# Kernel tuning notes

Measured on AMD Instinct MI355X. Metric: run time of the kernel, lower is better.

Reference implementation:

```python
import jax, jax.numpy as jnp
import numpy as np

N_TOKEN = 267735
D_EMBED = 1024
D_PROJ = 1024
DIV_VAL = 4
CUTOFFS = [20000, 40000, 200000, N_TOKEN]   # cutoffs + [n_token]
ENDS = [0] + CUTOFFS                         # cutoff_ends
N_CLUSTERS = len(CUTOFFS) - 1                # 3
HEAD_SIZE = CUTOFFS[0] + N_CLUSTERS          # 20003
N = 1024                                     # len*bsz


def setup_inputs() -> dict:
    key = jax.random.key(0)
    ks = jax.random.split(key, 16)
    d_embs = [D_EMBED // DIV_VAL ** i for i in range(4)]  # 1024,256,64,16
    sizes = [HEAD_SIZE] + [ENDS[i + 1] - ENDS[i] for i in range(1, 4)]  # 20003,20000,160000,67735
    s = 0.02
    inp = {
        'hidden': jax.random.normal(ks[0], (N, D_PROJ), dtype=jnp.float32),
        'target': jax.random.randint(ks[1], (N,), 0, N_TOKEN, dtype=jnp.int32),
    }
    for i in range(4):
        inp[f'w{i}'] = jax.random.normal(ks[2 + 3 * i], (sizes[i], d_embs[i]), dtype=jnp.float32) * s
        inp[f'b{i}'] = jnp.zeros((sizes[i],), dtype=jnp.float32)
        inp[f'p{i}'] = jax.random.normal(ks[3 + 3 * i], (D_PROJ, d_embs[i]), dtype=jnp.float32) * s
    return inp


def _logit(h, w, b, p):
    # F.linear(hidden, proj.t()) -> h @ p ; F.linear(., weight, bias) -> @ w.T + b
    return (h @ p) @ w.T + b


def reference(hidden, target, w0, b0, p0, w1, b1, p1, w2, b2, p2, w3, b3, p3):
    head_lp = jax.nn.log_softmax(_logit(hidden, w0, b0, p0), axis=1)  # [N, HEAD_SIZE]
    tails = [(w1, b1, p1), (w2, b2, p2), (w3, b3, p3)]
    lps = []
    # shortlist cluster: gather target logprob directly from head
    t0 = jnp.clip(target, 0, CUTOFFS[0] - 1)
    lps.append(jnp.take_along_axis(head_lp, t0[:, None], axis=1)[:, 0])
    # tail clusters: small projected matmul + log_softmax + gather, combined with cluster logprob head_lp[:, -i]
    for i in range(1, 4):
        l, r = ENDS[i], ENDS[i + 1]
        ti = jnp.clip(target - l, 0, r - l - 1)
        tail_lp = jax.nn.log_softmax(_logit(hidden, *tails[i - 1]), axis=1)  # [N, r-l]
        lps.append(head_lp[:, -i] + jnp.take_along_axis(tail_lp, ti[:, None], axis=1)[:, 0])
    masks = [(target >= ENDS[i]) & (target < ENDS[i + 1]) for i in range(4)]
    logprob = jnp.select(masks, lps)
    return -logprob  # [N] per-token NLL, original order (keep_order=True)
```

## Files before the change

### kernel.cpp

```cpp
#include <hip/hip_runtime.h>
#include <hip/hip_bf16.h>
#include <math.h>

#define NTOK 1024
#define DPROJ 1024
#define PSTRIDE 1376
#define HEADS 20003
#define LOG2E 1.4426950408889634f
#define LN2   0.6931471805599453f
#define WSCALE (4.0f * LOG2E)
#define PSCALE 0.25f

typedef __attribute__((ext_vector_type(8))) short bf16x8;
typedef __attribute__((ext_vector_type(4))) float f32x4;
typedef long long i64;

__device__ __forceinline__ short f2bf(float f) {
    unsigned u = __float_as_uint(f);
    u += 0x7fffu + ((u >> 16) & 1u);
    return (short)(u >> 16);
}
__device__ __forceinline__ unsigned pk4fp8(float a, float b, float c, float d) {
    unsigned v = __builtin_amdgcn_cvt_pk_fp8_f32(a, b, 0, false);
    v = __builtin_amdgcn_cvt_pk_fp8_f32(c, d, v, true);
    return v;
}
__device__ __forceinline__ unsigned char fp8_1(float a) {
    return (unsigned char)(__builtin_amdgcn_cvt_pk_fp8_f32(a, a, 0, false) & 0xff);
}
__device__ __forceinline__ i64 wfrag(const float* wp) {
    float4 x = *(const float4*)(wp);
    float4 y = *(const float4*)(wp + 4);
    unsigned lo = pk4fp8(x.x * WSCALE, x.y * WSCALE, x.z * WSCALE, x.w * WSCALE);
    unsigned hi = pk4fp8(y.x * WSCALE, y.y * WSCALE, y.z * WSCALE, y.w * WSCALE);
    return (i64)(((unsigned long long)hi << 32) | lo);
}

__global__ __launch_bounds__(256) void prep(const float* __restrict__ hidden,
                                            const float* __restrict__ p0,
                                            const float* __restrict__ p1,
                                            const float* __restrict__ p2,
                                            const float* __restrict__ p3,
                                            short* __restrict__ hbP,
                                            short* __restrict__ pTbP0,
                                            short* __restrict__ pTbP1,
                                            short* __restrict__ pTbP2,
                                            short* __restrict__ pTbP3,
                                            float* __restrict__ sums,
                                            unsigned char* __restrict__ pk3) {
    __shared__ float tile[64][65];
    int bid = blockIdx.x, tid = threadIdx.x;
    if (bid == 416) {
        float4 z = {0.f, 0.f, 0.f, 0.f};
        #pragma unroll
        for (int i = 0; i < 4; ++i) *((float4*)sums + i * 256 + tid) = z;
        return;
    }
    if (bid == 417) {
        int4 z = {0, 0, 0, 0};
        #pragma unroll
        for (int i = 0; i < 8; ++i) *((int4*)pk3 + i * 256 + tid) = z;
        return;
    }
    if (bid < 64) {
        int tt = bid;
        #pragma unroll
        for (int q = 0; q < 8; ++q) {
            int fi = q * 256 + tid;
            int l = fi & 63;
            int row = tt * 16 + (l & 15);
            int kb = (fi >> 6) * 32 + (l >> 4) * 8;
            const float* hp = hidden + row * 1024 + kb;
            float4 x = *(const float4*)hp;
            float4 y = *(const float4*)(hp + 4);
            bf16x8 o;
            o[0]=f2bf(x.x); o[1]=f2bf(x.y); o[2]=f2bf(x.z); o[3]=f2bf(x.w);
            o[4]=f2bf(y.x); o[5]=f2bf(y.y); o[6]=f2bf(y.z); o[7]=f2bf(y.w);
            *(bf16x8*)(hbP + (size_t)tt * 16384 + fi * 8) = o;
        }
        return;
    }
    int lb = bid - 64;
    const float* p; short* dst; int d, kt, jb;
    if (lb < 256)      { p = p0; dst = pTbP0; d = 1024; kt = lb >> 4; jb = lb & 15; }
    else if (lb < 320) { lb -= 256; p = p1; dst = pTbP1; d = 256; kt = lb >> 2; jb = lb & 3; }
    else if (lb < 336) { lb -= 320; p = p2; dst = pTbP2; d = 64;  kt = lb; jb = 0; }
    else               { lb -= 336; p = p3; dst = pTbP3; d = 16;  kt = lb; jb = 0; }
    int k0 = kt * 64, j0 = jb * 64;
    int tx = tid & 63, ty = tid >> 6;
    #pragma unroll
    for (int rr = 0; rr < 16; ++rr) {
        int k = k0 + ty * 16 + rr;
        int j = j0 + tx;
        if (j < d) tile[ty * 16 + rr][tx] = p[k * d + j];
    }
    __syncthreads();
    int ch = tid >> 5;
    int jtl = ch >> 1, ksl = ch & 1;
    int jt = jb * 4 + jtl;
    if (jt * 16 < d) {
        #pragma unroll
        for (int li = 0; li < 2; ++li) {
            int l = (tid & 31) + li * 32;
            int jl = jtl * 16 + (l & 15);
            int kl = ksl * 32 + (l >> 4) * 8;
            bf16x8 o;
            #pragma unroll
            for (int e = 0; e < 8; ++e) o[e] = f2bf(tile[kl + e][jl]);
            *(bf16x8*)(dst + ((size_t)jt * 32 + kt * 2 + ksl) * 512 + l * 8) = o;
        }
    }
}

__global__ __launch_bounds__(256) void proj(const short* __restrict__ hbP,
                                            const short* __restrict__ pTbP0,
                                            const short* __restrict__ pTbP1,
                                            const short* __restrict__ pTbP2,
                                            const short* __restrict__ pTbP3,
                                            float* __restrict__ projf,
                                            unsigned char* __restrict__ pk0,
                                            unsigned char* __restrict__ pk1,
                                            unsigned char* __restrict__ pk2,
                                            unsigned char* __restrict__ pk3) {
    __shared__ float spackf[16][72];
    __shared__ unsigned char sp8[1024];
    int tt = blockIdx.x, jbG = blockIdx.y, tid = threadIdx.x;
    const short* pB; unsigned char* pkc; int d, KSp, coloff, jb;
    if (jbG < 16)      { pB = pTbP0; pkc = pk0; d = 1024; KSp = 32; coloff = 0;    jb = jbG; }
    else if (jbG < 20) { pB = pTbP1; pkc = pk1; d = 256;  KSp = 8;  coloff = 1024; jb = jbG - 16; }
    else if (jbG == 20){ pB = pTbP2; pkc = pk2; d = 64;   KSp = 2;  coloff = 1280; jb = 0; }
    else               { pB = pTbP3; pkc = pk3; d = 16;   KSp = 1;  coloff = 1344; jb = 0; }
    int w = tid >> 6, lane = tid & 63;
    int l16 = lane & 15, quad = lane >> 4;
    int jt = jb * 4 + w;
    if (jt * 16 < d) {
        const short* ap = hbP + ((size_t)tt * 32) * 512 + lane * 8;
        const short* bp = pB  + ((size_t)jt * 32) * 512 + lane * 8;
        f32x4 x0 = {0,0,0,0}, x1 = {0,0,0,0};
        #pragma unroll
        for (int ks = 0; ks < 16; ++ks) {
            bf16x8 a0 = *(const bf16x8*)(ap + ks * 512);
            bf16x8 b0 = *(const bf16x8*)(bp + ks * 512);
            bf16x8 a1 = *(const bf16x8*)(ap + (ks + 16) * 512);
            bf16x8 b1 = *(const bf16x8*)(bp + (ks + 16) * 512);
            x0 = __builtin_amdgcn_mfma_f32_16x16x32_bf16(a0, b0, x0, 0, 0, 0);
            x1 = __builtin_amdgcn_mfma_f32_16x16x32_bf16(a1, b1, x1, 0, 0, 0);
        }
        f32x4 acc = x0 + x1;
        int kk = w * 16 + l16;
        #pragma unroll
        for (int r = 0; r < 4; ++r) {
            int tok = quad * 4 + r;
            spackf[tok][kk] = acc[r];
            sp8[(kk >> 5) * 512 + ((kk & 31) >> 3) * 128 + tok * 8 + (kk & 7)] = fp8_1(acc[r] * PSCALE);
        }
    }
    __syncthreads();
    int j0g = jb * 64;
    int dcols = min(64, d - j0g);
    {
        int row = tid >> 4, cb = (tid & 15) * 4;
        if (cb < dcols) {
            float4 v = *(const float4*)&spackf[row][cb];
            *(float4*)&projf[(tt * 16 + row) * PSTRIDE + coloff + j0g + cb] = v;
        }
    }
    {
        int nbytes = 16 * dcols;
        if (tid * 4 < nbytes) {
            unsigned char* gdst = pkc + ((size_t)tt * KSp + (j0g >> 5)) * 512;
            *(unsigned*)(gdst + tid * 4) = *(const unsigned*)(sp8 + tid * 4);
        }
    }
}

__device__ __forceinline__ void stage16k(const unsigned char* g, unsigned char* l,
                                         int wave, int lane) {
    const unsigned char* gs = g + wave * 4096 + lane * 16;
    unsigned char* ls = l + wave * 4096;
    #pragma unroll
    for (int i = 0; i < 4; ++i)
        __builtin_amdgcn_global_load_lds(
            (const __attribute__((address_space(1))) unsigned*)(gs + i * 1024),
            (__attribute__((address_space(3))) unsigned*)(ls + i * 1024), 16, 0, 0);
}

__device__ __forceinline__ void lse_head(const float* __restrict__ w,
                                         const float* __restrict__ bias,
                                         const unsigned char* __restrict__ pk,
                                         float* __restrict__ sumrow, int bid,
                                         unsigned char (*sbuf)[16384], float* bsum) {
    int tid = threadIdx.x;
    int wave = tid >> 6, lane = tid & 63;
    int quad = lane >> 4, l16 = lane & 15;
    int v0 = bid * 128 + wave * 32;

    for (int i = tid; i < NTOK; i += 256) bsum[i] = 0.f;

    i64 areg[2][32];
    float bb[2][4];
    #pragma unroll
    for (int vt = 0; vt < 2; ++vt) {
        int va = v0 + vt * 16 + l16;
        #pragma unroll
        for (int ks = 0; ks < 32; ++ks) {
            areg[vt][ks] = (va < HEADS) ? wfrag(w + (long)va * 1024 + ks * 32 + quad * 8) : 0;
        }
        #pragma unroll
        for (int r = 0; r < 4; ++r) {
            int vb = v0 + vt * 16 + quad * 4 + r;
            bb[vt][r] = (vb < HEADS) ? bias[vb] * LOG2E : -1e30f;
        }
    }

    stage16k(pk, sbuf[0], wave, lane);
    __syncthreads();
    for (int tt = 0; tt < 64; ++tt) {
        if (tt < 63) stage16k(pk + (size_t)(tt + 1) * 16384, sbuf[(tt + 1) & 1], wave, lane);
        const unsigned char* sb = sbuf[tt & 1];
        f32x4 x0 = {0,0,0,0}, x1 = x0, x2 = x0, x3 = x0;
        #pragma unroll
        for (int j = 0; j < 16; ++j) {
            i64 b0 = *(const i64*)(sb + j * 512 + lane * 8);
            i64 b1 = *(const i64*)(sb + (j + 16) * 512 + lane * 8);
            x0 = __builtin_amdgcn_mfma_f32_16x16x32_fp8_fp8(areg[0][j],      b0, x0, 0, 0, 0);
            x1 = __builtin_amdgcn_mfma_f32_16x16x32_fp8_fp8(areg[0][j + 16], b1, x1, 0, 0, 0);
            x2 = __builtin_amdgcn_mfma_f32_16x16x32_fp8_fp8(areg[1][j],      b0, x2, 0, 0, 0);
            x3 = __builtin_amdgcn_mfma_f32_16x16x32_fp8_fp8(areg[1][j + 16], b1, x3, 0, 0, 0);
        }
        f32x4 a0 = x0 + x1, a1 = x2 + x3;
        float e0 = exp2f(a0[0] + bb[0][0]) + exp2f(a0[2] + bb[0][2]) +
                   exp2f(a1[0] + bb[1][0]) + exp2f(a1[2] + bb[1][2]);
        float e1 = exp2f(a0[1] + bb[0][1]) + exp2f(a0[3] + bb[0][3]) +
                   exp2f(a1[1] + bb[1][1]) + exp2f(a1[3] + bb[1][3]);
        float e = e0 + e1;
        e += __shfl_xor(e, 16, 64);
        e += __shfl_xor(e, 32, 64);
        if (lane < 16) atomicAdd(&bsum[tt * 16 + lane], e);
        __syncthreads();
    }
    for (int i = tid; i < NTOK; i += 256)
        atomicAdd(&sumrow[i], bsum[i]);
}

template <int KS, int VT>
__device__ __forceinline__ void lse_tail(const float* __restrict__ w,
                                         const float* __restrict__ bias,
                                         const unsigned char* __restrict__ pk,
                                         float* __restrict__ sumrow,
                                         int V, int D, int bid, float* bsum) {
    int tid = threadIdx.x;
    int wave = tid >> 6, lane = tid & 63;
    int quad = lane >> 4, l16 = lane & 15;
    int v0 = bid * (64 * VT) + wave * (16 * VT);

    for (int i = tid; i < NTOK; i += 256) bsum[i] = 0.f;
    __syncthreads();

    i64 areg[VT][KS];
    float bb[VT][4];
    #pragma unroll
    for (int vt = 0; vt < VT; ++vt) {
        int va = v0 + vt * 16 + l16;
        #pragma unroll
        for (int ks = 0; ks < KS; ++ks) {
            int k = ks * 32 + quad * 8;
            areg[vt][ks] = (va < V && k < D) ? wfrag(w + (long)va * D + k) : 0;
        }
        #pragma unroll
        for (int r = 0; r < 4; ++r) {
            int vb = v0 + vt * 16 + quad * 4 + r;
            bb[vt][r] = (vb < V) ? bias[vb] * LOG2E : -1e30f;
        }
    }

    const i64* base = (const i64*)pk;
    i64 bn[KS];
    #pragma unroll
    for (int k = 0; k < KS; ++k) bn[k] = base[k * 64 + lane];
    for (int tt = 0; tt < 64; ++tt) {
        i64 bc[KS];
        #pragma unroll
        for (int k = 0; k < KS; ++k) bc[k] = bn[k];
        if (tt < 63) {
            const i64* nb = base + (size_t)(tt + 1) * KS * 64;
            #pragma unroll
            for (int k = 0; k < KS; ++k) bn[k] = nb[k * 64 + lane];
        }
        float e0 = 0.f, e1 = 0.f;
        #pragma unroll
        for (int vt = 0; vt < VT; ++vt) {
            f32x4 acc;
            if constexpr (KS >= 2) {
                f32x4 y0 = {0,0,0,0}, y1 = {0,0,0,0};
                #pragma unroll
                for (int j = 0; j < KS / 2; ++j) {
                    y0 = __builtin_amdgcn_mfma_f32_16x16x32_fp8_fp8(areg[vt][j], bc[j], y0, 0, 0, 0);
                    y1 = __builtin_amdgcn_mfma_f32_16x16x32_fp8_fp8(areg[vt][KS/2 + j], bc[KS/2 + j], y1, 0, 0, 0);
                }
                acc = y0 + y1;
            } else {
                f32x4 y0 = {0,0,0,0};
                acc = __builtin_amdgcn_mfma_f32_16x16x32_fp8_fp8(areg[vt][0], bc[0], y0, 0, 0, 0);
            }
            e0 += exp2f(acc[0] + bb[vt][0]) + exp2f(acc[2] + bb[vt][2]);
            e1 += exp2f(acc[1] + bb[vt][1]) + exp2f(acc[3] + bb[vt][3]);
        }
        float e = e0 + e1;
        e += __shfl_xor(e, 16, 64);
        e += __shfl_xor(e, 32, 64);
        if (lane < 16) atomicAdd(&bsum[tt * 16 + lane], e);
    }
    __syncthreads();
    for (int i = tid; i < NTOK; i += 256)
        atomicAdd(&sumrow[i], bsum[i]);
}

#define NB0 157
#define NB1 79
#define NB2 625
#define NB3 265

__global__ __launch_bounds__(256, 2) void lse_all(const float* __restrict__ w0, const float* __restrict__ b0,
                                                  const float* __restrict__ w1, const float* __restrict__ b1,
                                                  const float* __restrict__ w2, const float* __restrict__ b2,
                                                  const float* __restrict__ w3, const float* __restrict__ b3,
                                                  const unsigned char* __restrict__ pk0,
                                                  const unsigned char* __restrict__ pk1,
                                                  const unsigned char* __restrict__ pk2,
                                                  const unsigned char* __restrict__ pk3,
                                                  float* __restrict__ sums) {
    __shared__ unsigned char sbuf[2][16384];
    __shared__ float bsum[NTOK];
    int bid = blockIdx.x;
    if (bid < NB0) {
        lse_head(w0, b0, pk0, sums, bid, sbuf, bsum);
    } else if (bid < NB0 + NB1) {
        lse_tail<8, 4>(w1, b1, pk1, sums + NTOK,     20000,  256, bid - NB0, bsum);
    } else if (bid < NB0 + NB1 + NB2) {
        lse_tail<2, 4>(w2, b2, pk2, sums + 2 * NTOK, 160000, 64,  bid - NB0 - NB1, bsum);
    } else {
        lse_tail<1, 4>(w3, b3, pk3, sums + 3 * NTOK, 67735,  16,  bid - NB0 - NB1 - NB2, bsum);
    }
}

__global__ __launch_bounds__(256) void finalize(const int* __restrict__ target,
                                                const float* __restrict__ projf,
                                                const float* __restrict__ sums,
                                                const float* __restrict__ w0, const float* __restrict__ b0,
                                                const float* __restrict__ w1, const float* __restrict__ b1,
                                                const float* __restrict__ w2, const float* __restrict__ b2,
                                                const float* __restrict__ w3, const float* __restrict__ b3,
                                                float* __restrict__ out) {
    int wave = threadIdx.x >> 6, lane = threadIdx.x & 63;
    int row = blockIdx.x * 4 + wave;
    int t = target[row];
    int c = (t < 20000) ? 0 : (t < 40000) ? 1 : (t < 200000) ? 2 : 3;
    int col0 = (c == 0) ? t : (HEADS - c);
    const float* pr = projf + row * PSTRIDE;

    float s = 0.f;
    for (int k = lane; k < DPROJ; k += 64) s += pr[k] * w0[col0 * DPROJ + k];
    #pragma unroll
    for (int off = 32; off; off >>= 1) s += __shfl_xor(s, off, 64);
    float hl = s + b0[col0];
    float lse0 = __log2f(sums[row]) * LN2;

    float res;
    if (c == 0) {
        res = lse0 - hl;
    } else {
        const float* wc; const float* bc; int d, coloff, l;
        if (c == 1)      { wc = w1; bc = b1; d = 256; coloff = 1024; l = 20000; }
        else if (c == 2) { wc = w2; bc = b2; d = 64;  coloff = 1280; l = 40000; }
        else             { wc = w3; bc = b3; d = 16;  coloff = 1344; l = 200000; }
        int tc = t - l;
        float s2 = 0.f;
        for (int k = lane; k < d; k += 64) s2 += pr[coloff + k] * wc[tc * d + k];
        #pragma unroll
        for (int off = 32; off; off >>= 1) s2 += __shfl_xor(s2, off, 64);
        float tl = s2 + bc[tc];
        float lsec = __log2f(sums[c * NTOK + row]) * LN2;
        res = lse0 - hl + lsec - tl;
    }
    if (lane == 0) out[row] = res;
}


extern "C" void kernel_launch(void* const* d_in, const int* in_sizes, int n_in,
                              void* d_out, int out_size, void* d_ws, size_t ws_size,
                              hipStream_t stream) {
    const float* hidden = (const float*)d_in[0];
    const int*   target = (const int*)d_in[1];
    const float* w0 = (const float*)d_in[2];
    const float* b0 = (const float*)d_in[3];
    const float* p0 = (const float*)d_in[4];
    const float* w1 = (const float*)d_in[5];
    const float* b1 = (const float*)d_in[6];
    const float* p1 = (const float*)d_in[7];
    const float* w2 = (const float*)d_in[8];
    const float* b2 = (const float*)d_in[9];
    const float* p2 = (const float*)d_in[10];
    const float* w3 = (const float*)d_in[11];
    const float* b3 = (const float*)d_in[12];
    const float* p3 = (const float*)d_in[13];

    short* base = (short*)d_ws;
    short* hbP   = base;
    short* pTbP0 = base + 1048576;
    short* pTbP1 = base + 2097152;
    short* pTbP2 = base + 2359296;
    short* pTbP3 = base + 2424832;
    float* projf = (float*)((char*)d_ws + 4882432);
    unsigned char* pk0 = (unsigned char*)d_ws + 10518528;
    unsigned char* pk1 = pk0 + 1048576;
    unsigned char* pk2 = pk1 + 262144;
    unsigned char* pk3 = pk2 + 65536;
    float* sums  = (float*)((char*)d_ws + 11927552);

    prep<<<418, 256, 0, stream>>>(hidden, p0, p1, p2, p3,
                                  hbP, pTbP0, pTbP1, pTbP2, pTbP3, sums, pk3);
    proj<<<dim3(64, 22), 256, 0, stream>>>(hbP, pTbP0, pTbP1, pTbP2, pTbP3,
                                           projf, pk0, pk1, pk2, pk3);
    lse_all<<<NB0 + NB1 + NB2 + NB3, 256, 0, stream>>>(w0, b0, w1, b1, w2, b2, w3, b3,
                                                       pk0, pk1, pk2, pk3, sums);
    finalize<<<256, 256, 0, stream>>>(target, projf, sums,
                                      w0, b0, w1, b1, w2, b2, w3, b3, (float*)d_out);
}
```

Baseline: 349.8 us.

## Precompute exp of biases, write per-block partial sums, add reduction kernel

```diff
diff --git a/kernel.cpp b/kernel.cpp
--- a/kernel.cpp
+++ b/kernel.cpp
@@ -11,6 +11,14 @@
 #define WSCALE (4.0f * LOG2E)
 #define PSCALE 0.25f
 
+#if __has_builtin(__builtin_amdgcn_exp2f)
+#define EXP2(x) __builtin_amdgcn_exp2f(x)
+#else
+#define EXP2(x) exp2f(x)
+#endif
+
+#define MFMA8(a, b, c) __builtin_amdgcn_mfma_f32_16x16x32_fp8_fp8(a, b, c, 0, 0, 0)
+
 typedef __attribute__((ext_vector_type(8))) short bf16x8;
 typedef __attribute__((ext_vector_type(4))) float f32x4;
 typedef long long i64;
@@ -36,20 +44,56 @@
     return (i64)(((unsigned long long)hi << 32) | lo);
 }
 
+#define NB0 157
+#define NB1 79
+#define NB2 625
+#define NB3 265
+#define NBTOT (NB0 + NB1 + NB2 + NB3)
+
+#define EB0N 20096
+#define EB1N 20224
+#define EB2N 160000
+#define EB3N 67840
+#define EBTOT (EB0N + EB1N + EB2N + EB3N)
+
 __global__ __launch_bounds__(256) void prep(const float* __restrict__ hidden,
                                             const float* __restrict__ p0,
                                             const float* __restrict__ p1,
                                             const float* __restrict__ p2,
                                             const float* __restrict__ p3,
+                                            const float* __restrict__ b0,
+                                            const float* __restrict__ b1,
+                                            const float* __restrict__ b2,
+                                            const float* __restrict__ b3,
                                             short* __restrict__ hbP,
                                             short* __restrict__ pTbP0,
                                             short* __restrict__ pTbP1,
                                             short* __restrict__ pTbP2,
                                             short* __restrict__ pTbP3,
                                             float* __restrict__ sums,
-                                            unsigned char* __restrict__ pk3) {
+                                            unsigned char* __restrict__ pk3,
+                                            float* __restrict__ eb0,
+                                            float* __restrict__ eb1,
+                                            float* __restrict__ eb2,
+                                            float* __restrict__ eb3) {
     __shared__ float tile[64][65];
     int bid = blockIdx.x, tid = threadIdx.x;
+    if (bid >= 418) {
+        int g = (bid - 418) * 256 + tid;
+        if (g < EB0N) {
+            eb0[g] = (g < HEADS) ? exp2f(b0[g] * LOG2E) : 0.f;
+        } else if (g < EB0N + EB1N) {
+            int i = g - EB0N;
+            eb1[i] = (i < 20000) ? exp2f(b1[i] * LOG2E) : 0.f;
+        } else if (g < EB0N + EB1N + EB2N) {
+            int i = g - EB0N - EB1N;
+            eb2[i] = exp2f(b2[i] * LOG2E);
+        } else if (g < EBTOT) {
+            int i = g - EB0N - EB1N - EB2N;
+            eb3[i] = (i < 67735) ? exp2f(b3[i] * LOG2E) : 0.f;
+        }
+        return;
+    }
     if (bid == 416) {
         float4 z = {0.f, 0.f, 0.f, 0.f};
         #pragma unroll
@@ -186,9 +230,9 @@
 }
 
 __device__ __forceinline__ void lse_head(const float* __restrict__ w,
-                                         const float* __restrict__ bias,
+                                         const float* __restrict__ eb,
                                          const unsigned char* __restrict__ pk,
-                                         float* __restrict__ sumrow, int bid,
+                                         float* __restrict__ part, int bid,
                                          unsigned char (*sbuf)[16384], float* bsum) {
     int tid = threadIdx.x;
     int wave = tid >> 6, lane = tid & 63;
@@ -198,7 +242,7 @@
     for (int i = tid; i < NTOK; i += 256) bsum[i] = 0.f;
 
     i64 areg[2][32];
-    float bb[2][4];
+    float ee[2][4];
     #pragma unroll
     for (int vt = 0; vt < 2; ++vt) {
         int va = v0 + vt * 16 + l16;
@@ -207,10 +251,8 @@
             areg[vt][ks] = (va < HEADS) ? wfrag(w + (long)va * 1024 + ks * 32 + quad * 8) : 0;
         }
         #pragma unroll
-        for (int r = 0; r < 4; ++r) {
-            int vb = v0 + vt * 16 + quad * 4 + r;
-            bb[vt][r] = (vb < HEADS) ? bias[vb] * LOG2E : -1e30f;
-        }
+        for (int r = 0; r < 4; ++r)
+            ee[vt][r] = eb[v0 + vt * 16 + quad * 4 + r];
     }
 
     stage16k(pk, sbuf[0], wave, lane);
@@ -219,35 +261,36 @@
         if (tt < 63) stage16k(pk + (size_t)(tt + 1) * 16384, sbuf[(tt + 1) & 1], wave, lane);
         const unsigned char* sb = sbuf[tt & 1];
         f32x4 x0 = {0,0,0,0}, x1 = x0, x2 = x0, x3 = x0;
+        __builtin_amdgcn_s_setprio(1);
         #pragma unroll
         for (int j = 0; j < 16; ++j) {
             i64 b0 = *(const i64*)(sb + j * 512 + lane * 8);
             i64 b1 = *(const i64*)(sb + (j + 16) * 512 + lane * 8);
-            x0 = __builtin_amdgcn_mfma_f32_16x16x32_fp8_fp8(areg[0][j],      b0, x0, 0, 0, 0);
-            x1 = __builtin_amdgcn_mfma_f32_16x16x32_fp8_fp8(areg[0][j + 16], b1, x1, 0, 0, 0);
-            x2 = __builtin_amdgcn_mfma_f32_16x16x32_fp8_fp8(areg[1][j],      b0, x2, 0, 0, 0);
-            x3 = __builtin_amdgcn_mfma_f32_16x16x32_fp8_fp8(areg[1][j + 16], b1, x3, 0, 0, 0);
-        }
+            x0 = MFMA8(areg[0][j],      b0, x0);
+            x1 = MFMA8(areg[0][j + 16], b1, x1);
+            x2 = MFMA8(areg[1][j],      b0, x2);
+            x3 = MFMA8(areg[1][j + 16], b1, x3);
+        }
+        __builtin_amdgcn_s_setprio(0);
         f32x4 a0 = x0 + x1, a1 = x2 + x3;
-        float e0 = exp2f(a0[0] + bb[0][0]) + exp2f(a0[2] + bb[0][2]) +
-                   exp2f(a1[0] + bb[1][0]) + exp2f(a1[2] + bb[1][2]);
-        float e1 = exp2f(a0[1] + bb[0][1]) + exp2f(a0[3] + bb[0][3]) +
-                   exp2f(a1[1] + bb[1][1]) + exp2f(a1[3] + bb[1][3]);
+        float e0 = EXP2(a0[0]) * ee[0][0], e1 = EXP2(a0[1]) * ee[0][1];
+        e0 += EXP2(a0[2]) * ee[0][2];  e1 += EXP2(a0[3]) * ee[0][3];
+        e0 += EXP2(a1[0]) * ee[1][0];  e1 += EXP2(a1[1]) * ee[1][1];
+        e0 += EXP2(a1[2]) * ee[1][2];  e1 += EXP2(a1[3]) * ee[1][3];
         float e = e0 + e1;
         e += __shfl_xor(e, 16, 64);
         e += __shfl_xor(e, 32, 64);
         if (lane < 16) atomicAdd(&bsum[tt * 16 + lane], e);
         __syncthreads();
     }
-    for (int i = tid; i < NTOK; i += 256)
-        atomicAdd(&sumrow[i], bsum[i]);
+    *((float4*)part + tid) = *((const float4*)bsum + tid);
 }
 
 template <int KS, int VT>
 __device__ __forceinline__ void lse_tail(const float* __restrict__ w,
-                                         const float* __restrict__ bias,
+                                         const float* __restrict__ eb,
                                          const unsigned char* __restrict__ pk,
-                                         float* __restrict__ sumrow,
+                                         float* __restrict__ part,
                                          int V, int D, int bid, float* bsum) {
     int tid = threadIdx.x;
     int wave = tid >> 6, lane = tid & 63;
@@ -258,7 +301,7 @@
     __syncthreads();
 
     i64 areg[VT][KS];
-    float bb[VT][4];
+    float ee[VT][4];
     #pragma unroll
     for (int vt = 0; vt < VT; ++vt) {
         int va = v0 + vt * 16 + l16;
@@ -268,10 +311,8 @@
             areg[vt][ks] = (va < V && k < D) ? wfrag(w + (long)va * D + k) : 0;
         }
         #pragma unroll
-        for (int r = 0; r < 4; ++r) {
-            int vb = v0 + vt * 16 + quad * 4 + r;
-            bb[vt][r] = (vb < V) ? bias[vb] * LOG2E : -1e30f;
-        }
+        for (int r = 0; r < 4; ++r)
+            ee[vt][r] = eb[v0 + vt * 16 + quad * 4 + r];
     }
 
     const i64* base = (const i64*)pk;
@@ -287,24 +328,36 @@
             #pragma unroll
             for (int k = 0; k < KS; ++k) bn[k] = nb[k * 64 + lane];
         }
-        float e0 = 0.f, e1 = 0.f;
+        f32x4 accs[VT];
+        __builtin_amdgcn_s_setprio(1);
         #pragma unroll
         for (int vt = 0; vt < VT; ++vt) {
-            f32x4 acc;
-            if constexpr (KS >= 2) {
+            if constexpr (KS >= 4) {
                 f32x4 y0 = {0,0,0,0}, y1 = {0,0,0,0};
                 #pragma unroll
                 for (int j = 0; j < KS / 2; ++j) {
-                    y0 = __builtin_amdgcn_mfma_f32_16x16x32_fp8_fp8(areg[vt][j], bc[j], y0, 0, 0, 0);
-                    y1 = __builtin_amdgcn_mfma_f32_16x16x32_fp8_fp8(areg[vt][KS/2 + j], bc[KS/2 + j], y1, 0, 0, 0);
+                    y0 = MFMA8(areg[vt][j],          bc[j],          y0);
+                    y1 = MFMA8(areg[vt][KS/2 + j],   bc[KS/2 + j],   y1);
                 }
-                acc = y0 + y1;
+                accs[vt] = y0 + y1;
+            } else if constexpr (KS == 2) {
+                f32x4 y = {0,0,0,0};
+                y = MFMA8(areg[vt][0], bc[0], y);
+                y = MFMA8(areg[vt][1], bc[1], y);
+                accs[vt] = y;
             } else {
-                f32x4 y0 = {0,0,0,0};
-                acc = __builtin_amdgcn_mfma_f32_16x16x32_fp8_fp8(areg[vt][0], bc[0], y0, 0, 0, 0);
+                f32x4 y = {0,0,0,0};
+                accs[vt] = MFMA8(areg[vt][0], bc[0], y);
             }
-            e0 += exp2f(acc[0] + bb[vt][0]) + exp2f(acc[2] + bb[vt][2]);
-            e1 += exp2f(acc[1] + bb[vt][1]) + exp2f(acc[3] + bb[vt][3]);
+        }
+        __builtin_amdgcn_s_setprio(0);
+        float e0 = 0.f, e1 = 0.f;
+        #pragma unroll
+        for (int vt = 0; vt < VT; ++vt) {
+            e0 += EXP2(accs[vt][0]) * ee[vt][0];
+            e1 += EXP2(accs[vt][1]) * ee[vt][1];
+            e0 += EXP2(accs[vt][2]) * ee[vt][2];
+            e1 += EXP2(accs[vt][3]) * ee[vt][3];
         }
         float e = e0 + e1;
         e += __shfl_xor(e, 16, 64);
@@ -312,36 +365,53 @@
         if (lane < 16) atomicAdd(&bsum[tt * 16 + lane], e);
     }
     __syncthreads();
-    for (int i = tid; i < NTOK; i += 256)
-        atomicAdd(&sumrow[i], bsum[i]);
-}
-
-#define NB0 157
-#define NB1 79
-#define NB2 625
-#define NB3 265
-
-__global__ __launch_bounds__(256, 2) void lse_all(const float* __restrict__ w0, const float* __restrict__ b0,
-                                                  const float* __restrict__ w1, const float* __restrict__ b1,
-                                                  const float* __restrict__ w2, const float* __restrict__ b2,
-                                                  const float* __restrict__ w3, const float* __restrict__ b3,
+    *((float4*)part + tid) = *((const float4*)bsum + tid);
+}
+
+__global__ __launch_bounds__(256, 2) void lse_all(const float* __restrict__ w0, const float* __restrict__ eb0,
+                                                  const float* __restrict__ w1, const float* __restrict__ eb1,
+                                                  const float* __restrict__ w2, const float* __restrict__ eb2,
+                                                  const float* __restrict__ w3, const float* __restrict__ eb3,
                                                   const unsigned char* __restrict__ pk0,
                                                   const unsigned char* __restrict__ pk1,
                                                   const unsigned char* __restrict__ pk2,
                                                   const unsigned char* __restrict__ pk3,
-                                                  float* __restrict__ sums) {
+                                                  float* __restrict__ part) {
     __shared__ unsigned char sbuf[2][16384];
     __shared__ float bsum[NTOK];
     int bid = blockIdx.x;
+    float* slab = part + (size_t)bid * NTOK;
     if (bid < NB0) {
-        lse_head(w0, b0, pk0, sums, bid, sbuf, bsum);
+        lse_head(w0, eb0, pk0, slab, bid, sbuf, bsum);
     } else if (bid < NB0 + NB1) {
-        lse_tail<8, 4>(w1, b1, pk1, sums + NTOK,     20000,  256, bid - NB0, bsum);
+        lse_tail<8, 4>(w1, eb1, pk1, slab, 20000,  256, bid - NB0, bsum);
     } else if (bid < NB0 + NB1 + NB2) {
-        lse_tail<2, 4>(w2, b2, pk2, sums + 2 * NTOK, 160000, 64,  bid - NB0 - NB1, bsum);
+        lse_tail<2, 4>(w2, eb2, pk2, slab, 160000, 64,  bid - NB0 - NB1, bsum);
     } else {
-        lse_tail<1, 4>(w3, b3, pk3, sums + 3 * NTOK, 67735,  16,  bid - NB0 - NB1 - NB2, bsum);
-    }
+        lse_tail<1, 4>(w3, eb3, pk3, slab, 67735,  16,  bid - NB0 - NB1 - NB2, bsum);
+    }
+}
+
+__global__ __launch_bounds__(256) void reduce_part(const float* __restrict__ part,
+                                                   float* __restrict__ sums) {
+    int bid = blockIdx.x;
+    int c = bid >> 5, rem = bid & 31, q = rem >> 3, sl = rem & 7;
+    const int off[4] = {0, NB0, NB0 + NB1, NB0 + NB1 + NB2};
+    const int cnt[4] = {NB0, NB1, NB2, NB3};
+    int tok = q * 256 + threadIdx.x;
+    const float* p = part + (size_t)off[c] * NTOK + tok;
+    int n = cnt[c];
+    float s0 = 0.f, s1 = 0.f, s2 = 0.f, s3 = 0.f;
+    int b = sl;
+    for (; b + 24 < n; b += 32) {
+        s0 += p[(size_t)b * NTOK];
+        s1 += p[(size_t)(b + 8) * NTOK];
+        s2 += p[(size_t)(b + 16) * NTOK];
+        s3 += p[(size_t)(b + 24) * NTOK];
+    }
+    for (; b < n; b += 8) s0 += p[(size_t)b * NTOK];
+    float s = (s0 + s1) + (s2 + s3);
+    atomicAdd(&sums[c * NTOK + tok], s);
 }
 
 __global__ __launch_bounds__(256) void finalize(const int* __restrict__ target,
@@ -417,13 +487,20 @@
     unsigned char* pk2 = pk1 + 262144;
     unsigned char* pk3 = pk2 + 65536;
     float* sums  = (float*)((char*)d_ws + 11927552);
-
-    prep<<<418, 256, 0, stream>>>(hidden, p0, p1, p2, p3,
-                                  hbP, pTbP0, pTbP1, pTbP2, pTbP3, sums, pk3);
+    float* part  = (float*)((char*)d_ws + 11943936);
+    float* eb0   = (float*)((char*)d_ws + 16556032);
+    float* eb1   = (float*)((char*)d_ws + 16636416);
+    float* eb2   = (float*)((char*)d_ws + 16717312);
+    float* eb3   = (float*)((char*)d_ws + 17357312);
+
+    prep<<<1466, 256, 0, stream>>>(hidden, p0, p1, p2, p3, b0, b1, b2, b3,
+                                   hbP, pTbP0, pTbP1, pTbP2, pTbP3, sums, pk3,
+                                   eb0, eb1, eb2, eb3);
     proj<<<dim3(64, 22), 256, 0, stream>>>(hbP, pTbP0, pTbP1, pTbP2, pTbP3,
                                            projf, pk0, pk1, pk2, pk3);
-    lse_all<<<NB0 + NB1 + NB2 + NB3, 256, 0, stream>>>(w0, b0, w1, b1, w2, b2, w3, b3,
-                                                       pk0, pk1, pk2, pk3, sums);
+    lse_all<<<NBTOT, 256, 0, stream>>>(w0, eb0, w1, eb1, w2, eb2, w3, eb3,
+                                       pk0, pk1, pk2, pk3, part);
+    reduce_part<<<128, 256, 0, stream>>>(part, sums);
     finalize<<<256, 256, 0, stream>>>(target, projf, sums,
                                       w0, b0, w1, b1, w2, b2, w3, b3, (float*)d_out);
 }
```

Result: faster. 323.6 us (-7.5%).
